# Optimization experiments

Hardware: AMD Instinct MI355X
Metric: run time of the kernel (lower is better)

Reference implementation:

```python
import jax, jax.numpy as jnp
import numpy as np

N_HEADS = 16
MAX_LEN = 1024


def setup_inputs() -> dict:
    key = jax.random.key(0)
    ks = jax.random.split(key, 6)
    B, T, C = 4, 1024, 1024
    scale = 0.02
    return {
        "x": jax.random.normal(ks[0], (B, T, C), dtype=jnp.float32),
        "qkv_w": jax.random.normal(ks[1], (3 * C, C), dtype=jnp.float32) * scale,
        "qkv_b": jax.random.normal(ks[2], (3 * C,), dtype=jnp.float32) * scale,
        "proj_w": jax.random.normal(ks[3], (C, C), dtype=jnp.float32) * scale,
        "proj_b": jax.random.normal(ks[4], (C,), dtype=jnp.float32) * scale,
        "rel_pos_emb": jax.random.normal(ks[5], (2 * MAX_LEN - 1, C), dtype=jnp.float32) * scale,
    }


def reference(x, qkv_w, qkv_b, proj_w, proj_b, rel_pos_emb):
    B, T, C = x.shape
    H = N_HEADS
    D = C // H
    # QKV projection: (B,T,3C) -> (3,B,H,T,D)
    qkv = (x @ qkv_w.T + qkv_b).reshape(B, T, 3, H, D)
    qkv = jnp.transpose(qkv, (2, 0, 3, 1, 4))
    q, k, v = qkv[0], qkv[1], qkv[2]
    # scores: (B,H,T,T)
    att = jnp.einsum("bhtd,bhsd->bhts", q, k) / np.sqrt(D).astype(np.float32)
    # Relative position bias: gather-then-sum == sum-then-gather over head_dim.
    # Pre-reduce table to (2*max_len-1, H) to avoid materializing (T,T,C).
    table = rel_pos_emb.reshape(2 * MAX_LEN - 1, H, D).sum(axis=-1)  # (2L-1, H)
    pos = jnp.arange(T)
    rel_idx = pos[:, None] - pos[None, :] + (MAX_LEN - 1)  # (T,T)
    bias = jnp.transpose(table[rel_idx], (2, 0, 1))  # (H,T,T)
    att = att + bias[None]
    # causal mask: positions j > i masked to -inf
    causal = pos[None, :] > pos[:, None]  # (T,T) True above diagonal
    att = jnp.where(causal[None, None], -jnp.inf, att)
    att = jax.nn.softmax(att, axis=-1)
    out = jnp.einsum("bhts,bhsd->bhtd", att, v)  # (B,H,T,D)
    out = jnp.transpose(out, (0, 2, 1, 3)).reshape(B, T, C)
    return out @ proj_w.T + proj_b
```

## Files before the change

kernel.cpp:

```cpp
#include <hip/hip_runtime.h>
#include <hip/hip_bf16.h>
#include <cstdint>


typedef __bf16 bf16x8 __attribute__((ext_vector_type(8)));
typedef float f32x4 __attribute__((ext_vector_type(4)));
typedef float f32x16 __attribute__((ext_vector_type(16)));

__device__ __forceinline__ float bf2f(unsigned short u) {
    return __uint_as_float(((unsigned)u) << 16);
}
__device__ __forceinline__ unsigned short f2bf(float f) {
    __hip_bfloat16 h = __float2bfloat16(f);
    return *reinterpret_cast<unsigned short*>(&h);
}
__device__ __forceinline__ unsigned pk2(float a, float b) {
    return (unsigned)f2bf(a) | ((unsigned)f2bf(b) << 16);
}
__device__ __forceinline__ int4 cvt8(float4 a, float4 b) {
    union { unsigned short s[8]; int4 v; } u;
    u.s[0] = f2bf(a.x); u.s[1] = f2bf(a.y); u.s[2] = f2bf(a.z); u.s[3] = f2bf(a.w);
    u.s[4] = f2bf(b.x); u.s[5] = f2bf(b.y); u.s[6] = f2bf(b.z); u.s[7] = f2bf(b.w);
    return u.v;
}

__device__ __forceinline__ void gload16(const void* g, void* l) {
    __builtin_amdgcn_global_load_lds(
        reinterpret_cast<const __attribute__((address_space(1))) unsigned int*>(
            reinterpret_cast<uintptr_t>(g)),
        reinterpret_cast<__attribute__((address_space(3))) unsigned int*>(
            reinterpret_cast<uintptr_t>(l)),
        16, 0, 0);
}

__global__ __launch_bounds__(256) void cvt3(const float* __restrict__ x,
                                            const float* __restrict__ w1,
                                            const float* __restrict__ w2,
                                            unsigned short* __restrict__ ox,
                                            unsigned short* __restrict__ ow1,
                                            unsigned short* __restrict__ ow2) {
    const int i = blockIdx.x * 256 + threadIdx.x;
    const float* s; unsigned short* d; int li;
    if (i < 524288)      { s = x;  d = ox;  li = i; }
    else if (i < 917504) { s = w1; d = ow1; li = i - 524288; }
    else                 { s = w2; d = ow2; li = i - 917504; }
    const float4 a = *(const float4*)(s + (size_t)li * 8);
    const float4 b = *(const float4*)(s + (size_t)li * 8 + 4);
    *(int4*)(d + (size_t)li * 8) = cvt8(a, b);
}

__global__ __launch_bounds__(1024) void table_reduce(const float* __restrict__ rel,
                                                     float* __restrict__ table) {
    const int p = blockIdx.x;
    const int w = threadIdx.x >> 6, lane = threadIdx.x & 63;
    float v = rel[(size_t)p * 1024 + w * 64 + lane];
#pragma unroll
    for (int o = 32; o; o >>= 1) v += __shfl_xor(v, o, 64);
    if (lane == 0) table[p * 16 + w] = v;
}

#define GSTEP(AS_, BS_)                                                       \
    do {                                                                      \
        bf16x8 af[4], bfr[2];                                                 \
        _Pragma("unroll")                                                     \
        for (int r = 0; r < 4; ++r)                                           \
            af[r] = *(const bf16x8*)(&AS_[(64 * wr + 16 * r + lm) * 32 + quad * 8]); \
        _Pragma("unroll")                                                     \
        for (int c = 0; c < 2; ++c)                                           \
            bfr[c] = *(const bf16x8*)(&BS_[(32 * wc + 16 * c + lm) * 32 + quad * 8]); \
        _Pragma("unroll")                                                     \
        for (int r = 0; r < 4; ++r)                                           \
            _Pragma("unroll")                                                 \
            for (int c = 0; c < 2; ++c)                                       \
                acc[r][c] = __builtin_amdgcn_mfma_f32_16x16x32_bf16(af[r], bfr[c], acc[r][c], 0, 0, 0); \
    } while (0)

template <int EPI>
__global__ __launch_bounds__(512) void gemm_bt(const unsigned short* __restrict__ A,
                                               const unsigned short* __restrict__ B,
                                               const float* __restrict__ bias,
                                               unsigned short* __restrict__ outb,
                                               float* __restrict__ outf,
                                               int M, int N, int K) {
    __shared__ __attribute__((aligned(16))) unsigned short As0[128 * 32];
    __shared__ __attribute__((aligned(16))) unsigned short Bs0[128 * 32];
    __shared__ __attribute__((aligned(16))) unsigned short As1[128 * 32];
    __shared__ __attribute__((aligned(16))) unsigned short Bs1[128 * 32];
    const int bm = blockIdx.x * 128, bn = blockIdx.y * 128;
    const int tid = threadIdx.x, lane = tid & 63, wave = tid >> 6;
    const int wr = wave & 1, wc = wave >> 1;
    const int quad = lane >> 4, lm = lane & 15;

    const int srow = tid >> 2;
    const int scol = (tid & 3) * 8;
    const unsigned short* Ap = A + (size_t)(bm + srow) * K + scol;
    const unsigned short* Bp = B + (size_t)(bn + srow) * K + scol;
    unsigned short* AsW0 = &As0[tid * 8];
    unsigned short* BsW0 = &Bs0[tid * 8];
    unsigned short* AsW1 = &As1[tid * 8];
    unsigned short* BsW1 = &Bs1[tid * 8];

    f32x4 acc[4][2];
#pragma unroll
    for (int r = 0; r < 4; ++r)
#pragma unroll
        for (int c = 0; c < 2; ++c) acc[r][c] = (f32x4){0.f, 0.f, 0.f, 0.f};

    gload16(Ap, AsW0);
    gload16(Bp, BsW0);
    __syncthreads();

    for (int kk = 0; kk < K; kk += 64) {
        if (kk + 32 < K) {
            gload16(Ap + kk + 32, AsW1);
            gload16(Bp + kk + 32, BsW1);
        }
        GSTEP(As0, Bs0);
        __syncthreads();

        if (kk + 64 < K) {
            gload16(Ap + kk + 64, AsW0);
            gload16(Bp + kk + 64, BsW0);
        }
        GSTEP(As1, Bs1);
        __syncthreads();
    }

#pragma unroll
    for (int r = 0; r < 4; ++r)
#pragma unroll
        for (int c = 0; c < 2; ++c)
#pragma unroll
            for (int i = 0; i < 4; ++i) {
                const int row = bm + 64 * wr + 16 * r + quad * 4 + i;
                const int col = bn + 32 * wc + 16 * c + lm;
                const float v = acc[r][c][i] + bias[col];
                if (EPI == 0) {
                    const int b = row >> 10, t = row & 1023;
                    const int s3 = col >> 10, rem = col & 1023;
                    const int h = rem >> 6, d = rem & 63;
                    const size_t base = (((size_t)s3 * 4 + b) * 16 + h) * 65536;
                    const size_t off = base + (s3 == 2 ? (size_t)d * 1024 + t
                                                       : (size_t)t * 64 + d);
                    outb[off] = f2bf(v);
                } else {
                    outf[(size_t)row * N + col] = v;
                }
            }
}

#define LOADK(DST, KT)                                                        \
    do {                                                                      \
        const unsigned short* kr_ = Kg + (size_t)((KT) * 32 + l5) * 64 + hi8; \
        DST[0] = *(const bf16x8*)(kr_);                                       \
        DST[1] = *(const bf16x8*)(kr_ + 16);                                  \
        DST[2] = *(const bf16x8*)(kr_ + 32);                                  \
        DST[3] = *(const bf16x8*)(kr_ + 48);                                  \
    } while (0)

#define PACKP(p, BQA, BQB)                                                    \
    do {                                                                      \
        unsigned Q0 = pk2(p[0], p[1]),   Q1 = pk2(p[2], p[3]);                \
        unsigned Q2 = pk2(p[4], p[5]),   Q3 = pk2(p[6], p[7]);                \
        unsigned Q4 = pk2(p[8], p[9]),   Q5 = pk2(p[10], p[11]);              \
        unsigned Q6 = pk2(p[12], p[13]), Q7 = pk2(p[14], p[15]);              \
        asm volatile("v_permlane32_swap_b32 %0, %1" : "+v"(Q0), "+v"(Q2));    \
        asm volatile("v_permlane32_swap_b32 %0, %1" : "+v"(Q1), "+v"(Q3));    \
        asm volatile("v_permlane32_swap_b32 %0, %1" : "+v"(Q4), "+v"(Q6));    \
        asm volatile("v_permlane32_swap_b32 %0, %1" : "+v"(Q5), "+v"(Q7));    \
        BQA.w[0] = Q0;  BQA.w[1] = Q1;  BQA.w[2] = Q2;  BQA.w[3] = Q3;        \
        BQB.w[0] = Q4;  BQB.w[1] = Q5;  BQB.w[2] = Q6;  BQB.w[3] = Q7;        \
    } while (0)

#define ATTN_TILE(KF, KT)                                                     \
    do {                                                                      \
        const int jb = (KT) * 32;                                             \
        const unsigned short* vb_ = Vtg + (size_t)l5 * 1024 + jb + hi8;       \
        const bf16x8 vf00 = *(const bf16x8*)(vb_);                            \
        const bf16x8 vf01 = *(const bf16x8*)(vb_ + 16);                       \
        const bf16x8 vf10 = *(const bf16x8*)(vb_ + 32768);                    \
        const bf16x8 vf11 = *(const bf16x8*)(vb_ + 32768 + 16);               \
        f32x16 s = {0.f};                                                     \
        _Pragma("unroll")                                                     \
        for (int t = 0; t < 4; ++t)                                           \
            s = __builtin_amdgcn_mfma_f32_32x32x16_bf16(KF[t], qf[t], s, 0, 0, 0); \
        float p[16];                                                          \
        _Pragma("unroll")                                                     \
        for (int reg = 0; reg < 16; ++reg) {                                  \
            const int j = jb + (reg & 3) + 8 * (reg >> 2) + 4 * hi;           \
            p[reg] = fmaf(s[reg], 0.125f, tb[q - j + 127]);                   \
        }                                                                     \
        if (jb + 31 > qbase) {                                                \
            _Pragma("unroll")                                                 \
            for (int reg = 0; reg < 16; ++reg) {                              \
                const int j = jb + (reg & 3) + 8 * (reg >> 2) + 4 * hi;       \
                p[reg] = (j <= q) ? p[reg] : -1e30f;                          \
            }                                                                 \
        }                                                                     \
        float mx = p[0];                                                      \
        _Pragma("unroll")                                                     \
        for (int reg = 1; reg < 16; ++reg) mx = fmaxf(mx, p[reg]);            \
        mx = fmaxf(mx, __shfl_xor(mx, 32, 64));                               \
        if (!__all(mx <= mi + 8.f)) {                                         \
            const float mnew = fmaxf(mi, mx);                                 \
            const float alpha = __expf(mi - mnew);                            \
            mi = mnew;                                                        \
            li *= alpha;                                                      \
            _Pragma("unroll")                                                 \
            for (int reg = 0; reg < 16; ++reg) {                              \
                oa0[reg] *= alpha;                                            \
                oa1[reg] *= alpha;                                            \
            }                                                                 \
        }                                                                     \
        float lsum = 0.f;                                                     \
        _Pragma("unroll")                                                     \
        for (int reg = 0; reg < 16; ++reg) {                                  \
            p[reg] = __expf(p[reg] - mi);                                     \
            lsum += p[reg];                                                   \
        }                                                                     \
        li += lsum;                                                           \
        union { unsigned w[4]; bf16x8 v; } bq0, bq1;                          \
        PACKP(p, bq0, bq1);                                                   \
        oa0 = __builtin_amdgcn_mfma_f32_32x32x16_bf16(vf00, bq0.v, oa0, 0, 0, 0); \
        oa0 = __builtin_amdgcn_mfma_f32_32x32x16_bf16(vf01, bq1.v, oa0, 0, 0, 0); \
        oa1 = __builtin_amdgcn_mfma_f32_32x32x16_bf16(vf10, bq0.v, oa1, 0, 0, 0); \
        oa1 = __builtin_amdgcn_mfma_f32_32x32x16_bf16(vf11, bq1.v, oa1, 0, 0, 0); \
    } while (0)

#define ATTN_TILE2(KT)                                                        \
    do {                                                                      \
        const int jb = (KT) * 32;                                             \
        const unsigned short* vb_ = Vtg + (size_t)l5 * 1024 + jb + hi8;       \
        const bf16x8 vf00 = *(const bf16x8*)(vb_);                            \
        const bf16x8 vf01 = *(const bf16x8*)(vb_ + 16);                       \
        const bf16x8 vf02 = *(const bf16x8*)(vb_ + 32);                       \
        const bf16x8 vf03 = *(const bf16x8*)(vb_ + 48);                       \
        const bf16x8 vf10 = *(const bf16x8*)(vb_ + 32768);                    \
        const bf16x8 vf11 = *(const bf16x8*)(vb_ + 32768 + 16);               \
        const bf16x8 vf12 = *(const bf16x8*)(vb_ + 32768 + 32);               \
        const bf16x8 vf13 = *(const bf16x8*)(vb_ + 32768 + 48);               \
        f32x16 s0v = {0.f}, s1v = {0.f};                                      \
        _Pragma("unroll")                                                     \
        for (int t = 0; t < 4; ++t) {                                         \
            s0v = __builtin_amdgcn_mfma_f32_32x32x16_bf16(kA[t], qf[t], s0v, 0, 0, 0); \
            s1v = __builtin_amdgcn_mfma_f32_32x32x16_bf16(kB[t], qf[t], s1v, 0, 0, 0); \
        }                                                                     \
        if ((KT) + 2 < nt) LOADK(kA, (KT) + 2);                               \
        if ((KT) + 3 < nt) LOADK(kB, (KT) + 3);                               \
        float p0[16], p1[16];                                                 \
        _Pragma("unroll")                                                     \
        for (int reg = 0; reg < 16; ++reg) {                                  \
            const int jo = (reg & 3) + 8 * (reg >> 2) + 4 * hi;               \
            p0[reg] = fmaf(s0v[reg], 0.125f, tb[q - jb - jo + 127]);          \
            p1[reg] = fmaf(s1v[reg], 0.125f, tb[q - jb - 32 - jo + 127]);     \
        }                                                                     \
        if (jb + 63 > qbase) {                                                \
            _Pragma("unroll")                                                 \
            for (int reg = 0; reg < 16; ++reg) {                              \
                const int jo = (reg & 3) + 8 * (reg >> 2) + 4 * hi;           \
                p0[reg] = (jb + jo <= q) ? p0[reg] : -1e30f;                  \
                p1[reg] = (jb + 32 + jo <= q) ? p1[reg] : -1e30f;             \
            }                                                                 \
        }                                                                     \
        float mx = p0[0];                                                     \
        _Pragma("unroll")                                                     \
        for (int reg = 1; reg < 16; ++reg) mx = fmaxf(mx, p0[reg]);           \
        _Pragma("unroll")                                                     \
        for (int reg = 0; reg < 16; ++reg) mx = fmaxf(mx, p1[reg]);           \
        mx = fmaxf(mx, __shfl_xor(mx, 32, 64));                               \
        if (!__all(mx <= mi + 8.f)) {                                         \
            const float mnew = fmaxf(mi, mx);                                 \
            const float alpha = __expf(mi - mnew);                            \
            mi = mnew;                                                        \
            li *= alpha;                                                      \
            _Pragma("unroll")                                                 \
            for (int reg = 0; reg < 16; ++reg) {                              \
                oa0[reg] *= alpha;                                            \
                oa1[reg] *= alpha;                                            \
            }                                                                 \
        }                                                                     \
        float lsum = 0.f;                                                     \
        _Pragma("unroll")                                                     \
        for (int reg = 0; reg < 16; ++reg) {                                  \
            p0[reg] = __expf(p0[reg] - mi);                                   \
            p1[reg] = __expf(p1[reg] - mi);                                   \
            lsum += p0[reg] + p1[reg];                                        \
        }                                                                     \
        li += lsum;                                                           \
        union { unsigned w[4]; bf16x8 v; } bq00, bq01, bq10, bq11;            \
        PACKP(p0, bq00, bq01);                                                \
        PACKP(p1, bq10, bq11);                                                \
        oa0 = __builtin_amdgcn_mfma_f32_32x32x16_bf16(vf00, bq00.v, oa0, 0, 0, 0); \
        oa1 = __builtin_amdgcn_mfma_f32_32x32x16_bf16(vf10, bq00.v, oa1, 0, 0, 0); \
        oa0 = __builtin_amdgcn_mfma_f32_32x32x16_bf16(vf01, bq01.v, oa0, 0, 0, 0); \
        oa1 = __builtin_amdgcn_mfma_f32_32x32x16_bf16(vf11, bq01.v, oa1, 0, 0, 0); \
        oa0 = __builtin_amdgcn_mfma_f32_32x32x16_bf16(vf02, bq10.v, oa0, 0, 0, 0); \
        oa1 = __builtin_amdgcn_mfma_f32_32x32x16_bf16(vf12, bq10.v, oa1, 0, 0, 0); \
        oa0 = __builtin_amdgcn_mfma_f32_32x32x16_bf16(vf03, bq11.v, oa0, 0, 0, 0); \
        oa1 = __builtin_amdgcn_mfma_f32_32x32x16_bf16(vf13, bq11.v, oa1, 0, 0, 0); \
    } while (0)

__global__ __launch_bounds__(128) void attn_mfma(const unsigned short* __restrict__ qkvb,
                                                 const float* __restrict__ table,
                                                 unsigned short* __restrict__ y) {
    const int bh = blockIdx.x, b = bh >> 4, h = bh & 15;
    const int level = 15 - blockIdx.y;
    const int tid = threadIdx.x, lane = tid & 63, wave = tid >> 6;
    const int l5 = lane & 31, hi = lane >> 5, hi8 = hi * 8;

    __shared__ float tb[1152];

    const unsigned short* Qg  = qkvb + ((size_t)(b)*16 + h) * 65536;
    const unsigned short* Kg  = qkvb + ((size_t)(4 + b)*16 + h) * 65536;
    const unsigned short* Vtg = qkvb + ((size_t)(8 + b)*16 + h) * 65536;

    const int qbase = 64 * level + 32 * wave;
    const int q = qbase + l5;
    const int nt = 2 * level + wave + 1;

    bf16x8 qf[4];
    {
        const unsigned short* qr = Qg + (size_t)q * 64 + hi8;
#pragma unroll
        for (int t = 0; t < 4; ++t) qf[t] = *(const bf16x8*)(qr + t * 16);
    }

    const int tbn = 64 * level + 191;
    for (int i = tid; i < tbn; i += 128) tb[i] = table[(896 + i) * 16 + h];
    __syncthreads();

    f32x16 oa0 = {0.f}, oa1 = {0.f};
    float mi = -1e30f, li = 0.f;

    bf16x8 kA[4], kB[4];
    LOADK(kA, 0);
    LOADK(kB, nt > 1 ? 1 : 0);
    int kt = 0;
    for (; kt + 1 < nt; kt += 2) ATTN_TILE2(kt);
    if (kt < nt) ATTN_TILE(kA, kt);

    li += __shfl_xor(li, 32, 64);
    const float linv = 1.0f / li;
    unsigned short* yq = y + ((size_t)(b * 1024 + q)) * 1024 + h * 64;
#pragma unroll
    for (int g = 0; g < 4; ++g) {
        union { unsigned short u[4]; int2 v; } o4a, o4b;
#pragma unroll
        for (int i = 0; i < 4; ++i) {
            o4a.u[i] = f2bf(oa0[4 * g + i] * linv);
            o4b.u[i] = f2bf(oa1[4 * g + i] * linv);
        }
        *(int2*)(yq + 8 * g + 4 * hi) = o4a.v;
        *(int2*)(yq + 32 + 8 * g + 4 * hi) = o4b.v;
    }
}

extern "C" void kernel_launch(void* const* d_in, const int* in_sizes, int n_in,
                              void* d_out, int out_size, void* d_ws, size_t ws_size,
                              hipStream_t stream) {
    const float* x      = (const float*)d_in[0];
    const float* qkv_w  = (const float*)d_in[1];
    const float* qkv_b  = (const float*)d_in[2];
    const float* proj_w = (const float*)d_in[3];
    const float* proj_b = (const float*)d_in[4];
    const float* rel    = (const float*)d_in[5];
    float* out = (float*)d_out;

    char* ws = (char*)d_ws;
    unsigned short* xb   = (unsigned short*)(ws + 0);
    unsigned short* qwb  = (unsigned short*)(ws + 8388608);
    unsigned short* pwb  = (unsigned short*)(ws + 14680064);
    float* table         = (float*)(ws + 16777216);
    unsigned short* qkvb = (unsigned short*)(ws + 16908288);
    unsigned short* yb   = (unsigned short*)(ws + 42074112);

    cvt3<<<4096, 256, 0, stream>>>(x, qkv_w, proj_w, xb, qwb, pwb);
    table_reduce<<<2047, 1024, 0, stream>>>(rel, table);
    gemm_bt<0><<<dim3(32, 24), 512, 0, stream>>>(xb, qwb, qkv_b, qkvb, nullptr,
                                                 4096, 3072, 1024);
    attn_mfma<<<dim3(64, 16), 128, 0, stream>>>(qkvb, table, yb);
    gemm_bt<1><<<dim3(32, 8), 512, 0, stream>>>(yb, pwb, proj_b, nullptr, out,
                                                4096, 1024, 1024);
}
```

Measured before the change: 193.2 us.

## Triple-buffer GEMM LDS tiles with vmcnt-based waits instead of full syncs

The bf16 GEMM K-loop goes from double to triple buffering of the A and B LDS tiles, prefetching two stages ahead. The full __syncthreads after each step becomes an explicit s_waitcnt vmcnt(2) plus s_barrier, so one stage's loads can stay in flight across the barrier. This is meant to hide global-load latency behind the MFMA work. It costs extra LDS, which can lower occupancy, and the unrolled-by-3 loop with a fixed two-step tail assumes (K/32 - 2) is divisible by 3, which holds for K=1024.

Result: faster. 181.9 us (-5.9%).

```diff
diff --git a/kernel.cpp b/kernel.cpp
--- a/kernel.cpp
+++ b/kernel.cpp
@@ -75,6 +75,18 @@
                 acc[r][c] = __builtin_amdgcn_mfma_f32_16x16x32_bf16(af[r], bfr[c], acc[r][c], 0, 0, 0); \
     } while (0)
 
+#define PSTEP(ACUR, BCUR, APF, BPF, T)                                        \
+    do {                                                                      \
+        if ((T) + 2 < nst) {                                                  \
+            gload16(Ap + ((T) + 2) * 32, &APF[tid * 8]);                      \
+            gload16(Bp + ((T) + 2) * 32, &BPF[tid * 8]);                      \
+        }                                                                     \
+        GSTEP(ACUR, BCUR);                                                    \
+        asm volatile("s_waitcnt vmcnt(2)" ::: "memory");                      \
+        __builtin_amdgcn_s_barrier();                                         \
+        __builtin_amdgcn_sched_barrier(0);                                    \
+    } while (0)
+
 template <int EPI>
 __global__ __launch_bounds__(512) void gemm_bt(const unsigned short* __restrict__ A,
                                                const unsigned short* __restrict__ B,
@@ -86,6 +98,8 @@
     __shared__ __attribute__((aligned(16))) unsigned short Bs0[128 * 32];
     __shared__ __attribute__((aligned(16))) unsigned short As1[128 * 32];
     __shared__ __attribute__((aligned(16))) unsigned short Bs1[128 * 32];
+    __shared__ __attribute__((aligned(16))) unsigned short As2[128 * 32];
+    __shared__ __attribute__((aligned(16))) unsigned short Bs2[128 * 32];
     const int bm = blockIdx.x * 128, bn = blockIdx.y * 128;
     const int tid = threadIdx.x, lane = tid & 63, wave = tid >> 6;
     const int wr = wave & 1, wc = wave >> 1;
@@ -95,10 +109,7 @@
     const int scol = (tid & 3) * 8;
     const unsigned short* Ap = A + (size_t)(bm + srow) * K + scol;
     const unsigned short* Bp = B + (size_t)(bn + srow) * K + scol;
-    unsigned short* AsW0 = &As0[tid * 8];
-    unsigned short* BsW0 = &Bs0[tid * 8];
-    unsigned short* AsW1 = &As1[tid * 8];
-    unsigned short* BsW1 = &Bs1[tid * 8];
+    const int nst = K >> 5;
 
     f32x4 acc[4][2];
 #pragma unroll
@@ -106,25 +117,25 @@
 #pragma unroll
         for (int c = 0; c < 2; ++c) acc[r][c] = (f32x4){0.f, 0.f, 0.f, 0.f};
 
-    gload16(Ap, AsW0);
-    gload16(Bp, BsW0);
-    __syncthreads();
-
-    for (int kk = 0; kk < K; kk += 64) {
-        if (kk + 32 < K) {
-            gload16(Ap + kk + 32, AsW1);
-            gload16(Bp + kk + 32, BsW1);
-        }
-        GSTEP(As0, Bs0);
-        __syncthreads();
-
-        if (kk + 64 < K) {
-            gload16(Ap + kk + 64, AsW0);
-            gload16(Bp + kk + 64, BsW0);
-        }
-        GSTEP(As1, Bs1);
-        __syncthreads();
+    gload16(Ap, &As0[tid * 8]);
+    gload16(Bp, &Bs0[tid * 8]);
+    gload16(Ap + 32, &As1[tid * 8]);
+    gload16(Bp + 32, &Bs1[tid * 8]);
+    asm volatile("s_waitcnt vmcnt(2)" ::: "memory");
+    __builtin_amdgcn_s_barrier();
+    __builtin_amdgcn_sched_barrier(0);
+
+    int t = 0;
+    for (; t + 3 <= nst - 2; t += 3) {
+        PSTEP(As0, Bs0, As2, Bs2, t);
+        PSTEP(As1, Bs1, As0, Bs0, t + 1);
+        PSTEP(As2, Bs2, As1, Bs1, t + 2);
     }
+    GSTEP(As0, Bs0);
+    asm volatile("s_waitcnt vmcnt(0)" ::: "memory");
+    __builtin_amdgcn_s_barrier();
+    __builtin_amdgcn_sched_barrier(0);
+    GSTEP(As1, Bs1);
 
 #pragma unroll
     for (int r = 0; r < 4; ++r)
@@ -136,12 +147,12 @@
                 const int col = bn + 32 * wc + 16 * c + lm;
                 const float v = acc[r][c][i] + bias[col];
                 if (EPI == 0) {
-                    const int b = row >> 10, t = row & 1023;
+                    const int b = row >> 10, t2 = row & 1023;
                     const int s3 = col >> 10, rem = col & 1023;
                     const int h = rem >> 6, d = rem & 63;
                     const size_t base = (((size_t)s3 * 4 + b) * 16 + h) * 65536;
-                    const size_t off = base + (s3 == 2 ? (size_t)d * 1024 + t
-                                                       : (size_t)t * 64 + d);
+                    const size_t off = base + (s3 == 2 ? (size_t)d * 1024 + t2
+                                                       : (size_t)t2 * 64 + d);
                     outb[off] = f2bf(v);
                 } else {
                     outf[(size_t)row * N + col] = v;
```
